# Optimization experiments

Measured on AMD Instinct MI355X. Metric: run time of the kernel, lower is better.

The kernel has to match this reference:

```python
import math
import jax, jax.numpy as jnp
import numpy as np

B, N, C = 64, 1024, 128
RATIO = 0.5
EDGE_P = 0.02  # sparsity of the random binary adjacency


def setup_inputs() -> dict:
    key = jax.random.key(0)
    kx, ka, kw = jax.random.split(key, 3)
    x = jax.random.normal(kx, (B, N, C), dtype=jnp.float32)
    # binary adjacency (realistic graph input); module symmetrizes + clips anyway
    adj = (jax.random.uniform(ka, (B, N, N)) < EDGE_P).astype(jnp.float32)
    # TopKPooling learnable score weight (PyG initializes uniform; normal is fine for a baseline)
    w = jax.random.normal(kw, (C,), dtype=jnp.float32)
    return {"x": x, "adj": adj, "w": w}


def reference(x, adj, w):
    # x: [B, N, C], adj: [B, N, N], w: [C]
    b, n, c = x.shape
    k = int(math.ceil(RATIO * n))  # same k for every graph -> fully batched

    # per-sample: adj_tmp = adj + adj.T; adj_tmp[adj_tmp > 1] = 1
    a = adj + jnp.swapaxes(adj, 1, 2)
    a = jnp.minimum(a, 1.0)

    # TopKPooling score: tanh((x . w) / ||w||), select top-k nodes per graph
    score = jnp.tanh(jnp.einsum("bnc,c->bn", x, w) / jnp.linalg.norm(w))
    top_scores, perm = jax.lax.top_k(score, k)          # [B, k] each, descending

    # gated node features: x[perm] * score[perm]
    x_pool = jnp.take_along_axis(x, perm[..., None], axis=1) * top_scores[..., None]  # [B,k,C]

    # pooled dense adjacency: edges among selected nodes (to_dense_adj counts edges,
    # so entries are 1 where a nonzero edge existed) + 1 on diagonal from add_self_loops
    a_rows = jnp.take_along_axis(a, perm[:, :, None], axis=1)        # [B, k, N]
    a_sub = jnp.take_along_axis(a_rows, perm[:, None, :], axis=2)    # [B, k, k]
    adj_pooled = (a_sub != 0).astype(x.dtype) + jnp.eye(k, dtype=x.dtype)[None]

    return x_pool, adj_pooled
```

## Files before the change

### kernel.cpp

```cpp
#include <hip/hip_runtime.h>
#include <math.h>

#define NB 64
#define NN 1024
#define NC 128
#define NK 512

__global__ __launch_bounds__(1024) void scorerank_kernel(
    const float* __restrict__ x, const float* __restrict__ w,
    int* __restrict__ perm, float* __restrict__ gate, int* __restrict__ inv)
{
    __shared__ __align__(16) double s[NN];
    __shared__ int rp[1024];
    __shared__ double s_rnw;
    const int i = blockIdx.x;
    const int b = (i & 7) + ((i >> 5) << 3);
    const int q = (i >> 3) & 3;
    const int t = threadIdx.x;

    const int c0 = (t & 15) * 8;
    const float4 wa = *(const float4*)(w + c0);
    const float4 wb = *(const float4*)(w + c0 + 4);
    #pragma unroll 4
    for (int pass = 0; pass < 16; ++pass) {
        int row = pass * 64 + (t >> 4);
        const float* xr = x + ((size_t)b * NN + row) * NC + c0;
        float4 a  = *(const float4*)xr;
        float4 bb = *(const float4*)(xr + 4);
        double acc = (double)a.x * wa.x + (double)a.y * wa.y
                   + (double)a.z * wa.z + (double)a.w * wa.w
                   + (double)bb.x * wb.x + (double)bb.y * wb.y
                   + (double)bb.z * wb.z + (double)bb.w * wb.w;
        acc += __shfl_xor(acc, 1, 64);
        acc += __shfl_xor(acc, 2, 64);
        acc += __shfl_xor(acc, 4, 64);
        acc += __shfl_xor(acc, 8, 64);
        if ((t & 15) == 0) s[row] = acc;
    }
    if (t < 64) {
        double p = (double)w[t] * (double)w[t]
                 + (double)w[t + 64] * (double)w[t + 64];
        #pragma unroll
        for (int off = 32; off > 0; off >>= 1)
            p += __shfl_xor(p, off, 64);
        if (t == 0) s_rnw = 1.0 / sqrt(p);
    }
    __syncthreads();

    const int n  = q * 256 + (t & 255);
    const int jc = t >> 8;
    const double my = s[n];
    int r = 0;
    #pragma unroll 8
    for (int j = jc * 256; j < jc * 256 + 256; j += 2) {
        double2 o = *(const double2*)&s[j];
        r += (o.x > my) || ((o.x == my) && (j < n));
        r += (o.y > my) || ((o.y == my) && (j + 1 < n));
    }
    rp[t] = r;
    __syncthreads();
    if (jc == 0) {
        int rr = rp[t] + rp[t + 256] + rp[t + 512] + rp[t + 768];
        inv[b * NN + n] = (rr < NK) ? rr : -1;
        if (rr < NK) {
            perm[b * NK + rr] = n;
            gate[b * NK + rr] = (float)tanh(my * s_rnw);
        }
    }
}

__global__ __launch_bounds__(1024) void scan_xpool_kernel(
    const float* __restrict__ adj, const int* __restrict__ perm,
    const int* __restrict__ inv, const float* __restrict__ gate,
    const float* __restrict__ x, unsigned* __restrict__ bm,
    float* __restrict__ x_pool)
{
    __shared__ unsigned bits[64 * 17];
    __shared__ int sinv[NN];
    if (blockIdx.x >= 512) {
        int id = (blockIdx.x - 512) * 1024 + threadIdx.x;
        int c4 = id & (NC / 4 - 1);
        int bi = id >> 5;
        int b  = bi >> 9;
        int pi = perm[bi];
        float g = gate[bi];
        float4 v = *(const float4*)(x + ((size_t)b * NN + pi) * NC + c4 * 4);
        v.x *= g; v.y *= g; v.z *= g; v.w *= g;
        *(float4*)(x_pool + (size_t)id * 4) = v;
        return;
    }
    const int b = blockIdx.x >> 3;
    const int chunk = blockIdx.x & 7;
    const int t = threadIdx.x;
    for (int idx = t; idx < 64 * 17; idx += 1024) bits[idx] = 0;
    for (int idx = t; idx < NN; idx += 1024) sinv[idx] = inv[b * NN + idx];
    __syncthreads();

    const float* ab = adj + (size_t)b * NN * NN;
    const int* permb = perm + b * NK + chunk * 64;
    const int g  = t >> 8;
    const int lt = t & 255;

    int il = g;
    float4 v0 = *(const float4*)(ab + (size_t)permb[il] * NN + lt * 4);
    float4 v1 = *(const float4*)(ab + (size_t)permb[il + 4] * NN + lt * 4);
    float4 v2 = *(const float4*)(ab + (size_t)permb[il + 8] * NN + lt * 4);
    for (int it = 0; it < 16; ++it) {
        float4 vn = v0;
        if (it < 13)
            vn = *(const float4*)(ab + (size_t)permb[il + 12] * NN + lt * 4);
        #pragma unroll
        for (int u = 0; u < 4; ++u) {
            if (((const float*)&v0)[u] != 0.0f) {
                int j = sinv[lt * 4 + u];
                if (j >= 0)
                    atomicOr(&bits[il * 17 + (j >> 5)], 1u << (j & 31));
            }
        }
        v0 = v1; v1 = v2; v2 = vn; il += 4;
    }
    __syncthreads();
    {
        int dil = t & 63, w = t >> 6;
        if (t < 1024)
            bm[(size_t)b * 8192 + w * 512 + chunk * 64 + dil] = bits[dil * 17 + w];
    }
}

__global__ __launch_bounds__(1024) void adj_write_kernel(
    const unsigned* __restrict__ bm, float* __restrict__ out)
{
    __shared__ unsigned tcb[2 * 512];
    __shared__ unsigned fws[64 * 17];
    const int b = blockIdx.x >> 3;
    const int slab = blockIdx.x & 7;
    const int t = threadIdx.x;
    const unsigned* bmb = bm + (size_t)b * 8192;
    {
        int e = t >> 9, j = t & 511;
        tcb[t] = bmb[(slab * 2 + e) * 512 + j];
    }
    {
        int il = t & 63, wi = t >> 6;
        fws[il * 17 + wi] = bmb[wi * 512 + slab * 64 + il];
    }
    __syncthreads();

    float* ob = out + ((size_t)b * NK + slab * 64) * NK;
    #pragma unroll
    for (int it = 0; it < 8; ++it) {
        int lid = it * 1024 + t;
        int i_loc = lid >> 7;
        int i = slab * 64 + i_loc;
        int j4 = (lid & 127) * 4;
        unsigned fw = fws[i_loc * 17 + (j4 >> 5)];
        uint4 tq = *(const uint4*)&tcb[(i_loc >> 5) * 512 + j4];
        float4 res;
        float* rpn = (float*)&res;
        const unsigned* tp = (const unsigned*)&tq;
        #pragma unroll
        for (int e = 0; e < 4; ++e) {
            unsigned bit = ((fw >> ((j4 + e) & 31)) | (tp[e] >> (i & 31))) & 1u;
            float f = (float)bit;
            if (i == j4 + e) f += 1.0f;
            rpn[e] = f;
        }
        *(float4*)(ob + (size_t)i_loc * NK + j4) = res;
    }
}

extern "C" void kernel_launch(void* const* d_in, const int* in_sizes, int n_in,
                              void* d_out, int out_size, void* d_ws, size_t ws_size,
                              hipStream_t stream) {
    const float* x   = (const float*)d_in[0];
    const float* adj = (const float*)d_in[1];
    const float* w   = (const float*)d_in[2];
    float* out = (float*)d_out;

    char* p = (char*)d_ws;
    unsigned* bm   = (unsigned*)p;  p += sizeof(unsigned) * NB * 16 * NK;
    int*      perm = (int*)p;       p += sizeof(int) * NB * NK;
    float*    gate = (float*)p;     p += sizeof(float) * NB * NK;
    int*      inv  = (int*)p;

    float* x_pool     = out;
    float* adj_pooled = out + (size_t)NB * NK * NC;

    scorerank_kernel<<<NB * 4, 1024, 0, stream>>>(x, w, perm, gate, inv);
    scan_xpool_kernel<<<512 + NB * NK * NC / 4 / 1024, 1024, 0, stream>>>(
        adj, perm, inv, gate, x, bm, x_pool);
    adj_write_kernel<<<NB * 8, 1024, 0, stream>>>(bm, adj_pooled);
}
```

Measured before the change: 65.77 us.

## Fuse x_pool gather into score-rank kernel and deepen adjacency row prefetch

Moves the gated x_pool gather out of the adjacency scan kernel and into the score/rank kernel. Each block collects its selected nodes in shared memory and copies the corresponding x rows while they are likely still cache-resident. This removes 2048 extra blocks from the scan launch and a perm/gate reload. The adjacency scan prefetch pipeline is also deepened from three to four rows in flight, at the cost of more registers.

```diff
diff --git a/kernel.cpp b/kernel.cpp
--- a/kernel.cpp
+++ b/kernel.cpp
@@ -8,11 +8,15 @@
 
 __global__ __launch_bounds__(1024) void scorerank_kernel(
     const float* __restrict__ x, const float* __restrict__ w,
-    int* __restrict__ perm, float* __restrict__ gate, int* __restrict__ inv)
+    int* __restrict__ perm, float* __restrict__ gate, int* __restrict__ inv,
+    float* __restrict__ x_pool)
 {
     __shared__ __align__(16) double s[NN];
     __shared__ int rp[1024];
     __shared__ double s_rnw;
+    __shared__ int sel_nr[256];
+    __shared__ float sel_g[256];
+    __shared__ int scount;
     const int i = blockIdx.x;
     const int b = (i & 7) + ((i >> 5) << 3);
     const int q = (i >> 3) & 3;
@@ -45,6 +49,7 @@
             p += __shfl_xor(p, off, 64);
         if (t == 0) s_rnw = 1.0 / sqrt(p);
     }
+    if (t == 0) scount = 0;
     __syncthreads();
 
     const int n  = q * 256 + (t & 255);
@@ -63,32 +68,38 @@
         int rr = rp[t] + rp[t + 256] + rp[t + 512] + rp[t + 768];
         inv[b * NN + n] = (rr < NK) ? rr : -1;
         if (rr < NK) {
+            float gv = (float)tanh(my * s_rnw);
             perm[b * NK + rr] = n;
-            gate[b * NK + rr] = (float)tanh(my * s_rnw);
-        }
-    }
-}
-
-__global__ __launch_bounds__(1024) void scan_xpool_kernel(
+            gate[b * NK + rr] = gv;
+            int slot = atomicAdd(&scount, 1);
+            sel_nr[slot] = (n << 16) | rr;
+            sel_g[slot]  = gv;
+        }
+    }
+    __syncthreads();
+
+    const int cnt = scount;
+    const int rowSlot = t >> 5;
+    const int lane = t & 31;
+    for (int base = 0; base < cnt; base += 32) {
+        int idx = base + rowSlot;
+        if (idx < cnt) {
+            int nr = sel_nr[idx];
+            int n2 = nr >> 16, rr = nr & 0xffff;
+            float g = sel_g[idx];
+            float4 v = *(const float4*)(x + ((size_t)b * NN + n2) * NC + lane * 4);
+            v.x *= g; v.y *= g; v.z *= g; v.w *= g;
+            *(float4*)(x_pool + ((size_t)b * NK + rr) * NC + lane * 4) = v;
+        }
+    }
+}
+
+__global__ __launch_bounds__(1024) void adj_scan_kernel(
     const float* __restrict__ adj, const int* __restrict__ perm,
-    const int* __restrict__ inv, const float* __restrict__ gate,
-    const float* __restrict__ x, unsigned* __restrict__ bm,
-    float* __restrict__ x_pool)
+    const int* __restrict__ inv, unsigned* __restrict__ bm)
 {
     __shared__ unsigned bits[64 * 17];
     __shared__ int sinv[NN];
-    if (blockIdx.x >= 512) {
-        int id = (blockIdx.x - 512) * 1024 + threadIdx.x;
-        int c4 = id & (NC / 4 - 1);
-        int bi = id >> 5;
-        int b  = bi >> 9;
-        int pi = perm[bi];
-        float g = gate[bi];
-        float4 v = *(const float4*)(x + ((size_t)b * NN + pi) * NC + c4 * 4);
-        v.x *= g; v.y *= g; v.z *= g; v.w *= g;
-        *(float4*)(x_pool + (size_t)id * 4) = v;
-        return;
-    }
     const int b = blockIdx.x >> 3;
     const int chunk = blockIdx.x & 7;
     const int t = threadIdx.x;
@@ -105,10 +116,11 @@
     float4 v0 = *(const float4*)(ab + (size_t)permb[il] * NN + lt * 4);
     float4 v1 = *(const float4*)(ab + (size_t)permb[il + 4] * NN + lt * 4);
     float4 v2 = *(const float4*)(ab + (size_t)permb[il + 8] * NN + lt * 4);
+    float4 v3 = *(const float4*)(ab + (size_t)permb[il + 12] * NN + lt * 4);
     for (int it = 0; it < 16; ++it) {
         float4 vn = v0;
-        if (it < 13)
-            vn = *(const float4*)(ab + (size_t)permb[il + 12] * NN + lt * 4);
+        if (it < 12)
+            vn = *(const float4*)(ab + (size_t)permb[il + 16] * NN + lt * 4);
         #pragma unroll
         for (int u = 0; u < 4; ++u) {
             if (((const float*)&v0)[u] != 0.0f) {
@@ -117,13 +129,12 @@
                     atomicOr(&bits[il * 17 + (j >> 5)], 1u << (j & 31));
             }
         }
-        v0 = v1; v1 = v2; v2 = vn; il += 4;
+        v0 = v1; v1 = v2; v2 = v3; v3 = vn; il += 4;
     }
     __syncthreads();
     {
         int dil = t & 63, w = t >> 6;
-        if (t < 1024)
-            bm[(size_t)b * 8192 + w * 512 + chunk * 64 + dil] = bits[dil * 17 + w];
+        bm[(size_t)b * 8192 + w * 512 + chunk * 64 + dil] = bits[dil * 17 + w];
     }
 }
 
@@ -186,8 +197,7 @@
     float* x_pool     = out;
     float* adj_pooled = out + (size_t)NB * NK * NC;
 
-    scorerank_kernel<<<NB * 4, 1024, 0, stream>>>(x, w, perm, gate, inv);
-    scan_xpool_kernel<<<512 + NB * NK * NC / 4 / 1024, 1024, 0, stream>>>(
-        adj, perm, inv, gate, x, bm, x_pool);
+    scorerank_kernel<<<NB * 4, 1024, 0, stream>>>(x, w, perm, gate, inv, x_pool);
+    adj_scan_kernel<<<NB * 8, 1024, 0, stream>>>(adj, perm, inv, bm);
     adj_write_kernel<<<NB * 8, 1024, 0, stream>>>(bm, adj_pooled);
 }
```

New measurement: 66.26 us. Within noise of the previous version (+0.7%).
